# Optimization experiments

Hardware: AMD Instinct MI355X
Metric: run time of the kernel (lower is better)

## Reference

```python
import jax, jax.numpy as jnp
import numpy as np

D_MODEL = 1024

def setup_inputs() -> dict:
    key = jax.random.key(0)
    ks = jax.random.split(key, 7)
    x = jax.random.normal(ks[0], (4, 2048, D_MODEL), dtype=jnp.float32)
    s = 1.0 / np.sqrt(D_MODEL)
    Wq = jax.random.uniform(ks[1], (D_MODEL, D_MODEL), jnp.float32, -s, s)
    bq = jax.random.uniform(ks[2], (D_MODEL,), jnp.float32, -s, s)
    Wk = jax.random.uniform(ks[3], (D_MODEL, D_MODEL), jnp.float32, -s, s)
    bk = jax.random.uniform(ks[4], (D_MODEL,), jnp.float32, -s, s)
    Wv = jax.random.uniform(ks[5], (D_MODEL, D_MODEL), jnp.float32, -s, s)
    bv = jax.random.uniform(ks[6], (D_MODEL,), jnp.float32, -s, s)
    return {"x": x, "Wq": Wq, "bq": bq, "Wk": Wk, "bk": bk, "Wv": Wv, "bv": bv}

def reference(x, Wq, bq, Wk, bk, Wv, bv):
    # single-head self-attention: q,k,v are [B, S, D]
    q = x @ Wq + bq
    k = x @ Wk + bk
    v = x @ Wv + bv
    scale = 1.0 / jnp.sqrt(jnp.asarray(D_MODEL, x.dtype))
    scores = jnp.einsum('bsd,btd->bst', q, k) * scale  # [B, S, S]
    attn = jax.nn.softmax(scores, axis=-1)
    return jnp.einsum('bst,btd->bsd', attn, v)
```

## Files before the change

kernel.cpp:

```cpp
#include <hip/hip_runtime.h>
#include <hip/hip_bf16.h>
#include <stdint.h>


typedef __attribute__((ext_vector_type(8))) short short8;
typedef __attribute__((ext_vector_type(4))) float f32x4;

__device__ __forceinline__ unsigned short f2bf(float f) {
  union { float f; uint32_t u; } c; c.f = f;
  uint32_t u = c.u;
  u += 0x7FFFu + ((u >> 16) & 1u);
  return (unsigned short)(u >> 16);
}

__device__ __forceinline__ void gl16(const void* g, void* l) {
  __builtin_amdgcn_global_load_lds(
      (const __attribute__((address_space(1))) unsigned int*)g,
      (__attribute__((address_space(3))) unsigned int*)l, 16, 0, 0);
}

#define FENCE() asm volatile("" ::: "memory")
#define BARRIER() do { FENCE(); __builtin_amdgcn_s_barrier(); FENCE(); } while (0)
#define VMWAIT(n) asm volatile("s_waitcnt vmcnt(" #n ")" ::: "memory")

__global__ __launch_bounds__(512, 2) void k_qkv(
    const short* __restrict__ A, const short* __restrict__ B,
    short* __restrict__ Cb, short* __restrict__ vT,
    const float* __restrict__ b0, const float* __restrict__ b1,
    const float* __restrict__ b2)
{
  __shared__ short lds[65536];

  const int b = blockIdx.x;
  const int xcd = b & 7, r = b >> 3;
  const int tm = xcd * 4 + r / 12;
  const int zn = r % 12;
  const int z = zn >> 2, tn = zn & 3;

  const int tid = threadIdx.x;
  const int lane = tid & 63;
  const int wid = tid >> 6;
  const int fr = lane & 15, quad = lane >> 4, frk = fr & 7;
  const int wm = wid >> 2, wn = wid & 3;

  const long tileM = (long)tm * 256;
  const long tileN = (long)tn * 256;
  const short* Az = A;
  const short* Bz = B + (long)z * 1048576L;

  const int srow = tid >> 3;
  const int sslot = (tid & 7) ^ (srow & 7);
  const short* gA = Az + (tileM + srow) * 1024 + sslot * 8;
  const short* gB = Bz + (tileN + srow) * 1024 + sslot * 8;

  const int aBase = wm << 13;
  const int bBase = 16384 + (wn << 12);
  const int o0 = ((quad ^ frk) << 3) + (fr << 6);
  const int o1 = (((quad + 4) ^ frk) << 3) + (fr << 6);

  f32x4 acc[8][4] = {};

  auto stageA = [&](int tt) {
    const short* s = gA + tt * 64;
    short* d = &lds[(tt & 1) << 15];
    gl16(s,          d + (tid << 3));
    gl16(s + 65536,  d + 4096 + (tid << 3));
    gl16(s + 131072, d + 8192 + (tid << 3));
    gl16(s + 196608, d + 12288 + (tid << 3));
  };
  auto stageBh = [&](int tt, int h) {
    const short* s = gB + tt * 64 + h * 131072;
    short* d = &lds[((tt & 1) << 15) + 16384 + (h << 13)];
    gl16(s,         d + (tid << 3));
    gl16(s + 65536, d + 4096 + (tid << 3));
  };

  stageA(0); stageBh(0, 0); stageBh(0, 1); stageA(1);
  VMWAIT(4);
  BARRIER();

#pragma unroll 1
  for (int t = 0; t < 16; ++t) {
    const int bb = (t & 1) << 15;
    short8 af0[4][2], af1[4][2], bf0[2][2], bf1[2][2];

#pragma unroll
    for (int i = 0; i < 4; ++i) {
      af0[i][0] = *(const short8*)&lds[bb + aBase + (i << 10) + o0];
      af0[i][1] = *(const short8*)&lds[bb + aBase + (i << 10) + o1];
    }
#pragma unroll
    for (int j = 0; j < 2; ++j) {
      bf0[j][0] = *(const short8*)&lds[bb + bBase + (j << 10) + o0];
      bf0[j][1] = *(const short8*)&lds[bb + bBase + (j << 10) + o1];
    }
    if (t + 1 < 16) stageBh(t + 1, 0);
    BARRIER();
    __builtin_amdgcn_s_setprio(1);
#pragma unroll
    for (int i = 0; i < 4; ++i)
#pragma unroll
      for (int j = 0; j < 2; ++j) {
        acc[i][j] = __builtin_amdgcn_mfma_f32_16x16x32_bf16(af0[i][0], bf0[j][0], acc[i][j], 0, 0, 0);
        acc[i][j] = __builtin_amdgcn_mfma_f32_16x16x32_bf16(af0[i][1], bf0[j][1], acc[i][j], 0, 0, 0);
      }
    __builtin_amdgcn_s_setprio(0);
    BARRIER();

#pragma unroll
    for (int i = 0; i < 4; ++i) {
      af1[i][0] = *(const short8*)&lds[bb + aBase + ((i + 4) << 10) + o0];
      af1[i][1] = *(const short8*)&lds[bb + aBase + ((i + 4) << 10) + o1];
    }
    if (t + 1 < 16) stageBh(t + 1, 1);
    BARRIER();
    __builtin_amdgcn_s_setprio(1);
#pragma unroll
    for (int i = 0; i < 4; ++i)
#pragma unroll
      for (int j = 0; j < 2; ++j) {
        acc[i + 4][j] = __builtin_amdgcn_mfma_f32_16x16x32_bf16(af1[i][0], bf0[j][0], acc[i + 4][j], 0, 0, 0);
        acc[i + 4][j] = __builtin_amdgcn_mfma_f32_16x16x32_bf16(af1[i][1], bf0[j][1], acc[i + 4][j], 0, 0, 0);
      }
    __builtin_amdgcn_s_setprio(0);
    BARRIER();

#pragma unroll
    for (int j = 0; j < 2; ++j) {
      bf1[j][0] = *(const short8*)&lds[bb + bBase + ((j + 2) << 10) + o0];
      bf1[j][1] = *(const short8*)&lds[bb + bBase + ((j + 2) << 10) + o1];
    }
    BARRIER();
    __builtin_amdgcn_s_setprio(1);
#pragma unroll
    for (int i = 0; i < 4; ++i)
#pragma unroll
      for (int j = 0; j < 2; ++j) {
        acc[i + 4][j + 2] = __builtin_amdgcn_mfma_f32_16x16x32_bf16(af1[i][0], bf1[j][0], acc[i + 4][j + 2], 0, 0, 0);
        acc[i + 4][j + 2] = __builtin_amdgcn_mfma_f32_16x16x32_bf16(af1[i][1], bf1[j][1], acc[i + 4][j + 2], 0, 0, 0);
      }
    __builtin_amdgcn_s_setprio(0);
    BARRIER();

    if (t + 2 < 16) stageA(t + 2);
    BARRIER();
    __builtin_amdgcn_s_setprio(1);
#pragma unroll
    for (int i = 0; i < 4; ++i)
#pragma unroll
      for (int j = 0; j < 2; ++j) {
        acc[i][j + 2] = __builtin_amdgcn_mfma_f32_16x16x32_bf16(af0[i][0], bf1[j][0], acc[i][j + 2], 0, 0, 0);
        acc[i][j + 2] = __builtin_amdgcn_mfma_f32_16x16x32_bf16(af0[i][1], bf1[j][1], acc[i][j + 2], 0, 0, 0);
      }
    __builtin_amdgcn_s_setprio(0);
    if (t < 14) { VMWAIT(4); } else { VMWAIT(0); }
    BARRIER();
  }

  __syncthreads();
  short* scr = &lds[wid * 4608];
  if (z == 2) {
    const int gb = tm >> 3;
#pragma unroll
    for (int pass = 0; pass < 2; ++pass) {
#pragma unroll
      for (int j = 0; j < 4; ++j) {
        const float bv = b2[tileN + wn * 64 + j * 16 + fr];
#pragma unroll
        for (int i = 0; i < 4; ++i)
#pragma unroll
          for (int rr = 0; rr < 4; ++rr)
            scr[(j * 16 + fr) * 72 + i * 16 + quad * 4 + rr] =
                (short)f2bf(acc[pass * 4 + i][j][rr] + bv);
      }
      const long t0 = (long)(tm & 7) * 256 + wm * 128 + pass * 64;
#pragma unroll
      for (int c = 0; c < 8; ++c) {
        const int rr = c * 8 + (lane >> 3);
        const int cc = (lane & 7) * 8;
        short8 v = *(const short8*)&scr[rr * 72 + cc];
        const long gd = tileN + wn * 64 + rr;
        *(short8*)(vT + ((long)gb << 21) + gd * 2048 + t0 + cc) = v;
      }
      if (pass == 0) __syncthreads();
    }
  } else {
    short* C = Cb + (long)z * 8388608L;
    const float* bias = (z == 0) ? b0 : b1;
#pragma unroll
    for (int pass = 0; pass < 2; ++pass) {
#pragma unroll
      for (int j = 0; j < 4; ++j) {
        const float bv = bias[tileN + wn * 64 + j * 16 + fr];
#pragma unroll
        for (int i = 0; i < 4; ++i)
#pragma unroll
          for (int rr = 0; rr < 4; ++rr)
            scr[(i * 16 + quad * 4 + rr) * 72 + j * 16 + fr] =
                (short)f2bf(acc[pass * 4 + i][j][rr] + bv);
      }
#pragma unroll
      for (int c = 0; c < 8; ++c) {
        const int row = c * 8 + (lane >> 3);
        const int col = (lane & 7) * 8;
        short8 v = *(const short8*)&scr[row * 72 + col];
        *(short8*)(C + (tileM + wm * 128 + pass * 64 + row) * 1024 +
                   tileN + wn * 64 + col) = v;
      }
      if (pass == 0) __syncthreads();
    }
  }
}

__global__ __launch_bounds__(512, 2) void k_score(
    const short* __restrict__ A, const short* __restrict__ B,
    short* __restrict__ Pp, float scale, float* __restrict__ rowsum)
{
  __shared__ short lds[49152];

  const int b = blockIdx.x;
  const int xcd = b & 7, r = b >> 3;
  const int slab = xcd * 4 + (r >> 4);
  const int tn = r & 15;
  const int z = slab >> 3, tm = slab & 7;

  const int tid = threadIdx.x;
  const int lane = tid & 63;
  const int wid = tid >> 6;
  const int fr = lane & 15, quad = lane >> 4, frk = fr & 7;
  const int wm = wid >> 1, wn = wid & 1;

  const long tileM = (long)tm * 256;
  const long tileN = (long)tn * 128;
  const short* Az = A + (long)z * 2097152L;
  const short* Bz = B + (long)z * 2097152L;

  const int srow = tid >> 3;
  const int sslot = (tid & 7) ^ (srow & 7);
  const short* gA = Az + (tileM + srow) * 1024 + sslot * 8;
  const short* gB = Bz + (tileN + srow) * 1024 + sslot * 8;

  const int aBase = wm << 12;
  const int bBase = 16384 + (wn << 12);
  const int o0 = ((quad ^ frk) << 3) + (fr << 6);
  const int o1 = (((quad + 4) ^ frk) << 3) + (fr << 6);

  f32x4 acc[4][4] = {};

  auto stageA = [&](int tt) {
    const short* s = gA + tt * 64;
    short* d = &lds[(tt & 1) * 24576];
    gl16(s,          d + (tid << 3));
    gl16(s + 65536,  d + 4096 + (tid << 3));
    gl16(s + 131072, d + 8192 + (tid << 3));
    gl16(s + 196608, d + 12288 + (tid << 3));
  };
  auto stageB = [&](int tt) {
    const short* s = gB + tt * 64;
    short* d = &lds[(tt & 1) * 24576 + 16384];
    gl16(s,         d + (tid << 3));
    gl16(s + 65536, d + 4096 + (tid << 3));
  };

  stageA(0); stageB(0); stageA(1);
  VMWAIT(4);
  BARRIER();

#pragma unroll 1
  for (int t = 0; t < 16; ++t) {
    const int bb = (t & 1) * 24576;
    short8 af[4][2], bf0[2][2], bf1[2][2];

#pragma unroll
    for (int i = 0; i < 4; ++i) {
      af[i][0] = *(const short8*)&lds[bb + aBase + (i << 10) + o0];
      af[i][1] = *(const short8*)&lds[bb + aBase + (i << 10) + o1];
    }
#pragma unroll
    for (int j = 0; j < 2; ++j) {
      bf0[j][0] = *(const short8*)&lds[bb + bBase + (j << 10) + o0];
      bf0[j][1] = *(const short8*)&lds[bb + bBase + (j << 10) + o1];
    }
    if (t + 1 < 16) stageB(t + 1);
    BARRIER();
    __builtin_amdgcn_s_setprio(1);
#pragma unroll
    for (int i = 0; i < 4; ++i)
#pragma unroll
      for (int j = 0; j < 2; ++j) {
        acc[i][j] = __builtin_amdgcn_mfma_f32_16x16x32_bf16(af[i][0], bf0[j][0], acc[i][j], 0, 0, 0);
        acc[i][j] = __builtin_amdgcn_mfma_f32_16x16x32_bf16(af[i][1], bf0[j][1], acc[i][j], 0, 0, 0);
      }
    __builtin_amdgcn_s_setprio(0);
    BARRIER();

#pragma unroll
    for (int j = 0; j < 2; ++j) {
      bf1[j][0] = *(const short8*)&lds[bb + bBase + ((j + 2) << 10) + o0];
      bf1[j][1] = *(const short8*)&lds[bb + bBase + ((j + 2) << 10) + o1];
    }
    if (t + 2 < 16) stageA(t + 2);
    BARRIER();
    __builtin_amdgcn_s_setprio(1);
#pragma unroll
    for (int i = 0; i < 4; ++i)
#pragma unroll
      for (int j = 0; j < 2; ++j) {
        acc[i][j + 2] = __builtin_amdgcn_mfma_f32_16x16x32_bf16(af[i][0], bf1[j][0], acc[i][j + 2], 0, 0, 0);
        acc[i][j + 2] = __builtin_amdgcn_mfma_f32_16x16x32_bf16(af[i][1], bf1[j][1], acc[i][j + 2], 0, 0, 0);
      }
    __builtin_amdgcn_s_setprio(0);
    if (t < 14) { VMWAIT(4); } else { VMWAIT(0); }
    BARRIER();
  }

#pragma unroll
  for (int i = 0; i < 4; ++i)
#pragma unroll
    for (int j = 0; j < 4; ++j)
#pragma unroll
      for (int r = 0; r < 4; ++r)
        acc[i][j][r] = exp2f(acc[i][j][r] * scale);

  float* rsz = rowsum + (long)z * 2048 + tileM + wm * 64;
#pragma unroll
  for (int i = 0; i < 4; ++i)
#pragma unroll
    for (int r = 0; r < 4; ++r) {
      float s = acc[i][0][r] + acc[i][1][r] + acc[i][2][r] + acc[i][3][r];
      s += __shfl_xor(s, 1);
      s += __shfl_xor(s, 2);
      s += __shfl_xor(s, 4);
      s += __shfl_xor(s, 8);
      if (fr == 0) atomicAdd(&rsz[i * 16 + quad * 4 + r], s);
    }

  __syncthreads();
  short* C = Pp + (long)z * 4194304L;
  short* scr = &lds[wid * 4608];
#pragma unroll
  for (int j = 0; j < 4; ++j)
#pragma unroll
    for (int i = 0; i < 4; ++i)
#pragma unroll
      for (int r = 0; r < 4; ++r)
        scr[(i * 16 + quad * 4 + r) * 72 + j * 16 + fr] =
            (short)f2bf(acc[i][j][r]);
#pragma unroll
  for (int c = 0; c < 8; ++c) {
    const int row = c * 8 + (lane >> 3);
    const int col = (lane & 7) * 8;
    short8 v = *(const short8*)&scr[row * 72 + col];
    *(short8*)(C + (tileM + wm * 64 + row) * 2048 + tileN + wn * 64 + col) = v;
  }
}

__global__ __launch_bounds__(256) void k_pv(
    const short* __restrict__ A, const short* __restrict__ B,
    float* __restrict__ Cf, float* __restrict__ rowsum)
{
  const int b = blockIdx.x;
  const int s = b & 7, r0_ = b >> 3;
  const int z = r0_ >> 4;
  const int mem = r0_ & 15;
  const int tm = (s >> 1) * 4 + (mem >> 2);
  const int tn = (s & 1) * 4 + (mem & 3);

  __shared__ short lds[18432];

  const int tid  = threadIdx.x;
  const int lane = tid & 63;
  const int wid  = tid >> 6;
  const long tileM = (long)tm * 128;
  const long tileN = (long)tn * 128;
  const short* Az = A + (long)z * 4194304L;
  const short* Bz = B + (long)z * 2097152L;

  const int c0 = tid, c1 = 256 + tid;
  const short* gA0 = Az + (tileM + (c0 >> 2)) * 2048 + (c0 & 3) * 8;
  const short* gA1 = Az + (tileM + (c1 >> 2)) * 2048 + (c1 & 3) * 8;
  const short* gB0 = Bz + (tileN + (c0 >> 2)) * 2048 + (c0 & 3) * 8;
  const short* gB1 = Bz + (tileN + (c1 >> 2)) * 2048 + (c1 & 3) * 8;

  const int fr = lane & 15, quad = lane >> 4;
  const int waveM = (wid >> 1) * 64, waveN = (wid & 1) * 64;

  f32x4 acc[4][4] = {};

  {
    short* base = lds;
    gl16(gA0, base + c0 * 8);
    gl16(gA1, base + c1 * 8);
    gl16(gB0, base + 4096 + c0 * 8);
    gl16(gB1, base + 4096 + c1 * 8);
  }

  for (int t = 0; t < 64; ++t) {
    __syncthreads();
    if (t + 1 < 64) {
      const int kt = (t + 1) << 5;
      short* base = lds + ((t + 1) & 1) * 8192;
      gl16(gA0 + kt, base + c0 * 8);
      gl16(gA1 + kt, base + c1 * 8);
      gl16(gB0 + kt, base + 4096 + c0 * 8);
      gl16(gB1 + kt, base + 4096 + c1 * 8);
    }
    const short* sA = lds + (t & 1) * 8192;
    const short* sB = sA + 4096;
    short8 af[4], bf[4];
#pragma unroll
    for (int i = 0; i < 4; ++i)
      af[i] = *(const short8*)&sA[(waveM + i * 16 + fr) * 32 + quad * 8];
#pragma unroll
    for (int j = 0; j < 4; ++j)
      bf[j] = *(const short8*)&sB[(waveN + j * 16 + fr) * 32 + quad * 8];
#pragma unroll
    for (int i = 0; i < 4; ++i)
#pragma unroll
      for (int j = 0; j < 4; ++j)
        acc[i][j] = __builtin_amdgcn_mfma_f32_16x16x32_bf16(af[i], bf[j],
                                                            acc[i][j], 0, 0, 0);
  }

  float* C = Cf + (long)z * 2097152L;
#pragma unroll
  for (int i = 0; i < 4; ++i)
#pragma unroll
    for (int r = 0; r < 4; ++r) {
      const long gr = tileM + waveM + i * 16 + quad * 4 + r;
      const float rinv = 1.0f / rowsum[(long)z * 2048 + gr];
#pragma unroll
      for (int j = 0; j < 4; ++j)
        C[gr * 1024 + tileN + waveN + j * 16 + fr] = acc[i][j][r] * rinv;
    }
}

__global__ __launch_bounds__(256) void k_prep(
    const float4* __restrict__ x, ushort4* __restrict__ xb,
    const float* __restrict__ Wq, const float* __restrict__ Wk,
    const float* __restrict__ Wv, short* __restrict__ WT,
    float* __restrict__ rs)
{
  __shared__ short tile[32][33];
  const int b = blockIdx.x;
  if (b < 8192) {
    const long i = (long)b * 256 + threadIdx.x;
    float4 v = x[i];
    ushort4 o;
    o.x = f2bf(v.x); o.y = f2bf(v.y); o.z = f2bf(v.z); o.w = f2bf(v.w);
    xb[i] = o;
  } else if (b < 11264) {
    const int idx = b - 8192;
    const int z = idx >> 10, rem = idx & 1023;
    const float* W = (z == 0) ? Wq : ((z == 1) ? Wk : Wv);
    short* d = WT + (long)z * 1024 * 1024;
    const int n0 = (rem & 31) * 32, d0 = (rem >> 5) * 32;
    const int tx = threadIdx.x & 31, ty = threadIdx.x >> 5;
#pragma unroll
    for (int p = 0; p < 4; ++p)
      tile[ty + p * 8][tx] = (short)f2bf(W[(long)(d0 + ty + p * 8) * 1024 + n0 + tx]);
    __syncthreads();
#pragma unroll
    for (int p = 0; p < 4; ++p)
      d[(long)(n0 + ty + p * 8) * 1024 + d0 + tx] = tile[tx][ty + p * 8];
  } else {
#pragma unroll
    for (int p = 0; p < 32; ++p)
      rs[p * 256 + threadIdx.x] = 0.0f;
  }
}

extern "C" void kernel_launch(void* const* d_in, const int* in_sizes, int n_in,
                              void* d_out, int out_size, void* d_ws, size_t ws_size,
                              hipStream_t stream) {
  const float* x  = (const float*)d_in[0];
  const float* Wq = (const float*)d_in[1];
  const float* bq = (const float*)d_in[2];
  const float* Wk = (const float*)d_in[3];
  const float* bk = (const float*)d_in[4];
  const float* Wv = (const float*)d_in[5];
  const float* bv = (const float*)d_in[6];

  char* ws = (char*)d_ws;
  short* xb  = (short*)(ws);
  short* wt  = (short*)(ws + 16777216);
  short* qkv = (short*)(ws + 23068672);
  short* Pp  = (short*)(ws + 73400320);
  float* rs  = (float*)(ws + 106954752);
  short* vT  = qkv + 2L * 8388608;

  k_prep<<<11265, 256, 0, stream>>>((const float4*)x, (ushort4*)xb,
                                    Wq, Wk, Wv, wt, rs);
  k_qkv<<<384, 512, 0, stream>>>(xb, wt, qkv, vT, bq, bk, bv);
  k_score<<<512, 512, 0, stream>>>(qkv, qkv + 8388608, Pp,
                                   0.03125f * 1.44269504088896f, rs);
  k_pv<<<512, 256, 0, stream>>>(Pp, vT, (float*)d_out, rs);
}
```

Before: 251.4 us.

## Enlarge score kernel tile to 256x256 with 128x64 per-wave subtiles

The QK^T score kernel now computes a 256x256 output tile per block instead of 256x128, halving the grid to 256 blocks. Each of the 8 waves owns a 128x64 subtile, so the accumulators grow to 8x4 fragments. The B operand is staged in two halves and the MFMA phases are interleaved with LDS reads. The aim is to raise arithmetic intensity and cut redundant global and LDS traffic for Q/K operands, in exchange for more LDS (128KB), higher register pressure and fewer resident blocks, which leaves less room to hide latency.

```diff
diff --git a/kernel.cpp b/kernel.cpp
--- a/kernel.cpp
+++ b/kernel.cpp
@@ -216,22 +216,22 @@
     const short* __restrict__ A, const short* __restrict__ B,
     short* __restrict__ Pp, float scale, float* __restrict__ rowsum)
 {
-  __shared__ short lds[49152];
+  __shared__ short lds[65536];
 
   const int b = blockIdx.x;
-  const int xcd = b & 7, r = b >> 3;
-  const int slab = xcd * 4 + (r >> 4);
-  const int tn = r & 15;
-  const int z = slab >> 3, tm = slab & 7;
+  const int xcd = b & 7, jb = b >> 3;
+  const int p = xcd * 4 + (jb >> 3);
+  const int tn = jb & 7;
+  const int z = p >> 3, tm = p & 7;
 
   const int tid = threadIdx.x;
   const int lane = tid & 63;
   const int wid = tid >> 6;
-  const int fr = lane & 15, quad = lane >> 4, frk = fr & 7;
-  const int wm = wid >> 1, wn = wid & 1;
+  const int fr = lane & 15, quad = lane >> 4;
+  const int wm = wid >> 2, wn = wid & 3;
 
   const long tileM = (long)tm * 256;
-  const long tileN = (long)tn * 128;
+  const long tileN = (long)tn * 256;
   const short* Az = A + (long)z * 2097152L;
   const short* Bz = B + (long)z * 2097152L;
 
@@ -240,65 +240,96 @@
   const short* gA = Az + (tileM + srow) * 1024 + sslot * 8;
   const short* gB = Bz + (tileN + srow) * 1024 + sslot * 8;
 
-  const int aBase = wm << 12;
-  const int bBase = 16384 + (wn << 12);
+  const int frk = fr & 7;
+  const int aBase = wm << 13;
+  const int bRow  = 16384 + ((wn >> 1) << 13) + ((wn & 1) << 12);
   const int o0 = ((quad ^ frk) << 3) + (fr << 6);
   const int o1 = (((quad + 4) ^ frk) << 3) + (fr << 6);
 
-  f32x4 acc[4][4] = {};
+  f32x4 acc[8][4] = {};
 
   auto stageA = [&](int tt) {
     const short* s = gA + tt * 64;
-    short* d = &lds[(tt & 1) * 24576];
+    short* d = &lds[(tt & 1) << 15];
     gl16(s,          d + (tid << 3));
     gl16(s + 65536,  d + 4096 + (tid << 3));
     gl16(s + 131072, d + 8192 + (tid << 3));
     gl16(s + 196608, d + 12288 + (tid << 3));
   };
-  auto stageB = [&](int tt) {
-    const short* s = gB + tt * 64;
-    short* d = &lds[(tt & 1) * 24576 + 16384];
+  auto stageBh = [&](int tt, int h) {
+    const short* s = gB + tt * 64 + h * 131072;
+    short* d = &lds[((tt & 1) << 15) + 16384 + (h << 13)];
     gl16(s,         d + (tid << 3));
     gl16(s + 65536, d + 4096 + (tid << 3));
   };
 
-  stageA(0); stageB(0); stageA(1);
+  stageA(0); stageBh(0, 0); stageBh(0, 1); stageA(1);
   VMWAIT(4);
   BARRIER();
 
 #pragma unroll 1
   for (int t = 0; t < 16; ++t) {
-    const int bb = (t & 1) * 24576;
-    short8 af[4][2], bf0[2][2], bf1[2][2];
+    const int bb = (t & 1) << 15;
+    short8 af0[4][2], af1[4][2], bf0[2][2], bf1[2][2];
 
 #pragma unroll
     for (int i = 0; i < 4; ++i) {
-      af[i][0] = *(const short8*)&lds[bb + aBase + (i << 10) + o0];
-      af[i][1] = *(const short8*)&lds[bb + aBase + (i << 10) + o1];
+      af0[i][0] = *(const short8*)&lds[bb + aBase + (i << 10) + o0];
+      af0[i][1] = *(const short8*)&lds[bb + aBase + (i << 10) + o1];
     }
 #pragma unroll
     for (int j = 0; j < 2; ++j) {
-      bf0[j][0] = *(const short8*)&lds[bb + bBase + (j << 10) + o0];
-      bf0[j][1] = *(const short8*)&lds[bb + bBase + (j << 10) + o1];
-    }
-    if (t + 1 < 16) stageB(t + 1);
-    BARRIER();
-    __builtin_amdgcn_s_setprio(1);
-#pragma unroll
-    for (int i = 0; i < 4; ++i)
-#pragma unroll
-      for (int j = 0; j < 2; ++j) {
-        acc[i][j] = __builtin_amdgcn_mfma_f32_16x16x32_bf16(af[i][0], bf0[j][0], acc[i][j], 0, 0, 0);
-        acc[i][j] = __builtin_amdgcn_mfma_f32_16x16x32_bf16(af[i][1], bf0[j][1], acc[i][j], 0, 0, 0);
+      bf0[j][0] = *(const short8*)&lds[bb + bRow + (j << 10) + o0];
+      bf0[j][1] = *(const short8*)&lds[bb + bRow + (j << 10) + o1];
+    }
+    if (t + 1 < 16) stageBh(t + 1, 0);
+    BARRIER();
+    __builtin_amdgcn_s_setprio(1);
+#pragma unroll
+    for (int i = 0; i < 4; ++i)
+#pragma unroll
+      for (int j = 0; j < 2; ++j) {
+        acc[i][j] = __builtin_amdgcn_mfma_f32_16x16x32_bf16(af0[i][0], bf0[j][0], acc[i][j], 0, 0, 0);
+        acc[i][j] = __builtin_amdgcn_mfma_f32_16x16x32_bf16(af0[i][1], bf0[j][1], acc[i][j], 0, 0, 0);
+      }
+    __builtin_amdgcn_s_setprio(0);
+    BARRIER();
+
+#pragma unroll
+    for (int i = 0; i < 4; ++i) {
+      af1[i][0] = *(const short8*)&lds[bb + aBase + ((i + 4) << 10) + o0];
+      af1[i][1] = *(const short8*)&lds[bb + aBase + ((i + 4) << 10) + o1];
+    }
+    if (t + 1 < 16) stageBh(t + 1, 1);
+    BARRIER();
+    __builtin_amdgcn_s_setprio(1);
+#pragma unroll
+    for (int i = 0; i < 4; ++i)
+#pragma unroll
+      for (int j = 0; j < 2; ++j) {
+        acc[i + 4][j] = __builtin_amdgcn_mfma_f32_16x16x32_bf16(af1[i][0], bf0[j][0], acc[i + 4][j], 0, 0, 0);
+        acc[i + 4][j] = __builtin_amdgcn_mfma_f32_16x16x32_bf16(af1[i][1], bf0[j][1], acc[i + 4][j], 0, 0, 0);
       }
     __builtin_amdgcn_s_setprio(0);
     BARRIER();
 
 #pragma unroll
     for (int j = 0; j < 2; ++j) {
-      bf1[j][0] = *(const short8*)&lds[bb + bBase + ((j + 2) << 10) + o0];
-      bf1[j][1] = *(const short8*)&lds[bb + bBase + ((j + 2) << 10) + o1];
-    }
+      bf1[j][0] = *(const short8*)&lds[bb + bRow + ((j + 2) << 10) + o0];
+      bf1[j][1] = *(const short8*)&lds[bb + bRow + ((j + 2) << 10) + o1];
+    }
+    BARRIER();
+    __builtin_amdgcn_s_setprio(1);
+#pragma unroll
+    for (int i = 0; i < 4; ++i)
+#pragma unroll
+      for (int j = 0; j < 2; ++j) {
+        acc[i + 4][j + 2] = __builtin_amdgcn_mfma_f32_16x16x32_bf16(af1[i][0], bf1[j][0], acc[i + 4][j + 2], 0, 0, 0);
+        acc[i + 4][j + 2] = __builtin_amdgcn_mfma_f32_16x16x32_bf16(af1[i][1], bf1[j][1], acc[i + 4][j + 2], 0, 0, 0);
+      }
+    __builtin_amdgcn_s_setprio(0);
+    BARRIER();
+
     if (t + 2 < 16) stageA(t + 2);
     BARRIER();
     __builtin_amdgcn_s_setprio(1);
@@ -306,8 +337,8 @@
     for (int i = 0; i < 4; ++i)
 #pragma unroll
       for (int j = 0; j < 2; ++j) {
-        acc[i][j + 2] = __builtin_amdgcn_mfma_f32_16x16x32_bf16(af[i][0], bf1[j][0], acc[i][j + 2], 0, 0, 0);
-        acc[i][j + 2] = __builtin_amdgcn_mfma_f32_16x16x32_bf16(af[i][1], bf1[j][1], acc[i][j + 2], 0, 0, 0);
+        acc[i][j + 2] = __builtin_amdgcn_mfma_f32_16x16x32_bf16(af0[i][0], bf1[j][0], acc[i][j + 2], 0, 0, 0);
+        acc[i][j + 2] = __builtin_amdgcn_mfma_f32_16x16x32_bf16(af0[i][1], bf1[j][1], acc[i][j + 2], 0, 0, 0);
       }
     __builtin_amdgcn_s_setprio(0);
     if (t < 14) { VMWAIT(4); } else { VMWAIT(0); }
@@ -315,16 +346,16 @@
   }
 
 #pragma unroll
-  for (int i = 0; i < 4; ++i)
+  for (int i = 0; i < 8; ++i)
 #pragma unroll
     for (int j = 0; j < 4; ++j)
 #pragma unroll
       for (int r = 0; r < 4; ++r)
         acc[i][j][r] = exp2f(acc[i][j][r] * scale);
 
-  float* rsz = rowsum + (long)z * 2048 + tileM + wm * 64;
-#pragma unroll
-  for (int i = 0; i < 4; ++i)
+  float* rsz = rowsum + (long)z * 2048 + tileM + wm * 128;
+#pragma unroll
+  for (int i = 0; i < 8; ++i)
 #pragma unroll
     for (int r = 0; r < 4; ++r) {
       float s = acc[i][0][r] + acc[i][1][r] + acc[i][2][r] + acc[i][3][r];
@@ -339,19 +370,23 @@
   short* C = Pp + (long)z * 4194304L;
   short* scr = &lds[wid * 4608];
 #pragma unroll
-  for (int j = 0; j < 4; ++j)
-#pragma unroll
-    for (int i = 0; i < 4; ++i)
-#pragma unroll
-      for (int r = 0; r < 4; ++r)
-        scr[(i * 16 + quad * 4 + r) * 72 + j * 16 + fr] =
-            (short)f2bf(acc[i][j][r]);
-#pragma unroll
-  for (int c = 0; c < 8; ++c) {
-    const int row = c * 8 + (lane >> 3);
-    const int col = (lane & 7) * 8;
-    short8 v = *(const short8*)&scr[row * 72 + col];
-    *(short8*)(C + (tileM + wm * 64 + row) * 2048 + tileN + wn * 64 + col) = v;
+  for (int pass = 0; pass < 2; ++pass) {
+#pragma unroll
+    for (int j = 0; j < 4; ++j)
+#pragma unroll
+      for (int i = 0; i < 4; ++i)
+#pragma unroll
+        for (int r = 0; r < 4; ++r)
+          scr[(i * 16 + quad * 4 + r) * 72 + j * 16 + fr] =
+              (short)f2bf(acc[pass * 4 + i][j][r]);
+#pragma unroll
+    for (int c = 0; c < 8; ++c) {
+      const int row = c * 8 + (lane >> 3);
+      const int col = (lane & 7) * 8;
+      short8 v = *(const short8*)&scr[row * 72 + col];
+      *(short8*)(C + (tileM + wm * 128 + pass * 64 + row) * 2048 +
+                 tileN + wn * 64 + col) = v;
+    }
   }
 }
 
@@ -492,7 +527,7 @@
   k_prep<<<11265, 256, 0, stream>>>((const float4*)x, (ushort4*)xb,
                                     Wq, Wk, Wv, wt, rs);
   k_qkv<<<384, 512, 0, stream>>>(xb, wt, qkv, vT, bq, bk, bv);
-  k_score<<<512, 512, 0, stream>>>(qkv, qkv + 8388608, Pp,
-                                   0.03125f * 1.44269504088896f, rs);
+  k_score<<<256, 1024 / 2, 0, stream>>>(qkv, qkv + 8388608, Pp,
+                                        0.03125f * 1.44269504088896f, rs);
   k_pv<<<512, 256, 0, stream>>>(Pp, vT, (float*)d_out, rs);
 }
```

After: 248.5 us. About the same (-1.2%).
